# Performance work log

Measured on AMD Instinct MI355X. Metric: run time of the kernel, lower is better.

The kernel has to match this reference:

```python
import jax, jax.numpy as jnp
import numpy as np

B, S, D, H, HD, F = 2, 2048, 2048, 16, 128, 8192
EPS = 1e-6
NEG_INF = -1e10


def rmsnorm(x, scale, eps=EPS):
    # T5 LayerNorm: no centering, mean of squares, learned scale
    x = x.astype(jnp.float32)
    mean2 = jnp.mean(jnp.square(x), axis=-1, keepdims=True)
    return x * jax.lax.rsqrt(mean2 + eps) * scale


def setup_inputs() -> dict:
    key = jax.random.key(0)
    ks = jax.random.split(key, 10)
    sd = 0.02
    return {
        "x": jax.random.normal(ks[0], (B, S, D), jnp.float32),
        "ln1_scale": jnp.ones((D,), jnp.float32),
        "wq": jax.random.normal(ks[1], (D, H, HD), jnp.float32) * sd,
        "wk": jax.random.normal(ks[2], (D, H, HD), jnp.float32) * sd,
        "wv": jax.random.normal(ks[3], (D, H, HD), jnp.float32) * sd,
        "qln_scale": jnp.ones((HD,), jnp.float32),
        "kln_scale": jnp.ones((HD,), jnp.float32),
        "wo": jax.random.normal(ks[4], (H, HD, D), jnp.float32) * sd,
        "ln2_scale": jnp.ones((D,), jnp.float32),
        "wi0": jax.random.normal(ks[5], (D, F), jnp.float32) * sd,
        "wi1": jax.random.normal(ks[6], (D, F), jnp.float32) * sd,
        "wout": jax.random.normal(ks[7], (F, D), jnp.float32) * sd,
    }


def reference(x, ln1_scale, wq, wk, wv, qln_scale, kln_scale, wo, ln2_scale, wi0, wi1, wout):
    # ---- pre-attention RMSNorm ----
    lnx = rmsnorm(x, ln1_scale)                                  # [B,S,D]
    # ---- QKV projections (DenseGeneral D -> (H,HD)) ----
    q = jnp.einsum("bsd,dhk->bshk", lnx, wq)                      # [B,S,H,HD]
    k = jnp.einsum("bsd,dhk->bshk", lnx, wk)
    v = jnp.einsum("bsd,dhk->bshk", lnx, wv)
    # ---- fused per-head QK LayerNorm ----
    q = rmsnorm(q, qln_scale)
    k = rmsnorm(k, kln_scale)
    # ---- attention scores + causal bias + softmax ----
    logits = jnp.einsum("bqhd,bkhd->bhqk", q, k)                  # [B,H,S,S]
    causal = jnp.tril(jnp.ones((S, S), bool))
    bias = jnp.where(causal, 0.0, NEG_INF).astype(logits.dtype)  # [S,S]
    probs = jax.nn.softmax(logits + bias[None, None])             # [B,H,S,S]
    # ---- weighted values + output projection ----
    attn = jnp.einsum("bhqk,bkhd->bqhd", probs, v)                # [B,S,H,HD]
    attn_out = jnp.einsum("bqhd,hdm->bqm", attn, wo)              # [B,S,D]
    inter = x + attn_out
    # ---- pre-MLP RMSNorm + gated MLP (silu * linear) ----
    h = rmsnorm(inter, ln2_scale)
    g = jax.nn.silu(h @ wi0) * (h @ wi1)                          # [B,S,F]
    mlp_out = g @ wout                                            # [B,S,D]
    return inter + mlp_out
```

## Files before the change

kernel.cpp:

```cpp
#include <hip/hip_runtime.h>

typedef unsigned short u16;
typedef unsigned int u32;
typedef __attribute__((ext_vector_type(8))) short bf16x8;
typedef __attribute__((ext_vector_type(2))) float f32x2;
typedef __attribute__((ext_vector_type(4))) float f32x4;
typedef __attribute__((ext_vector_type(4))) u32 u32x4;

#define DEV __device__ __forceinline__

DEV u16 f2bf(float x) {
    u32 u = __builtin_bit_cast(u32, x);
    u += 0x7fffu + ((u >> 16) & 1u);
    return (u16)(u >> 16);
}
DEV float bf2f(u16 b) {
    u32 u = ((u32)b) << 16;
    return __builtin_bit_cast(float, u);
}

#define MFMA16(a, b, c) __builtin_amdgcn_mfma_f32_16x16x32_bf16((a), (b), (c), 0, 0, 0)

#define GLL16(gp, lp)                                                      \
    __builtin_amdgcn_global_load_lds(                                      \
        (const __attribute__((address_space(1))) u32*)(const void*)(gp),   \
        (__attribute__((address_space(3))) u32*)(void*)(lp), 16, 0, 0)

__global__ void fillsent(float* __restrict__ out, int n, float val)
{
    for (int i = blockIdx.x * blockDim.x + threadIdx.x; i < n; i += gridDim.x * blockDim.x)
        out[i] = val;
}

__global__ void wtrans(const float* __restrict__ in, u16* __restrict__ out, int K, int N)
{
    __shared__ u16 t[64][65];
    const int n0 = blockIdx.x * 64, k0 = blockIdx.y * 64, tid = threadIdx.x;
    for (int i = tid; i < 4096; i += 256) {
        int r = i >> 6, c = i & 63;
        t[r][c] = f2bf(in[(size_t)(k0 + r) * N + n0 + c]);
    }
    __syncthreads();
    for (int i = tid; i < 4096; i += 256) {
        int r = i >> 6, c = i & 63;
        out[(size_t)(n0 + r) * K + k0 + c] = t[c][r];
    }
}

__global__ void wtrans4(const float* __restrict__ s0, const float* __restrict__ s1,
                        const float* __restrict__ s2, const float* __restrict__ s3,
                        u16* __restrict__ d0, u16* __restrict__ d1,
                        u16* __restrict__ d2, u16* __restrict__ d3)
{
    const float* in;
    u16* out;
    switch (blockIdx.z) {
        case 0: in = s0; out = d0; break;
        case 1: in = s1; out = d1; break;
        case 2: in = s2; out = d2; break;
        default: in = s3; out = d3; break;
    }
    __shared__ u16 t[64][65];
    const int n0 = blockIdx.x * 64, k0 = blockIdx.y * 64, tid = threadIdx.x;
    for (int i = tid; i < 4096; i += 256) {
        int r = i >> 6, c = i & 63;
        t[r][c] = f2bf(in[(size_t)(k0 + r) * 2048 + n0 + c]);
    }
    __syncthreads();
    for (int i = tid; i < 4096; i += 256) {
        int r = i >> 6, c = i & 63;
        out[(size_t)(n0 + r) * 2048 + k0 + c] = t[c][r];
    }
}

__global__ void vtrans(const u16* __restrict__ in, u16* __restrict__ out)
{
    __shared__ u16 t[64][65];
    const int d0 = blockIdx.x * 64, s0 = blockIdx.y * 64, bh = blockIdx.z, tid = threadIdx.x;
    const u16* ip = in + (size_t)bh * 2048 * 128;
    u16* op = out + (size_t)bh * 128 * 2048;
    for (int i = tid; i < 4096; i += 256) {
        int r = i >> 6, c = i & 63;
        t[r][c] = ip[(size_t)(s0 + r) * 128 + d0 + c];
    }
    __syncthreads();
    for (int i = tid; i < 4096; i += 256) {
        int r = i >> 6, c = i & 63;
        op[(size_t)(d0 + r) * 2048 + s0 + c] = t[c][r];
    }
}

__global__ __launch_bounds__(256) void rmsnorm_d(const float* __restrict__ in,
                                                 const float* __restrict__ sc,
                                                 u16* __restrict__ out)
{
    __shared__ float red[4];
    const int row = blockIdx.x, tid = threadIdx.x;
    const float* p = in + (size_t)row * 2048 + tid * 8;
    f32x4 a = *(const f32x4*)p;
    f32x4 b = *(const f32x4*)(p + 4);
    float ss = a[0]*a[0] + a[1]*a[1] + a[2]*a[2] + a[3]*a[3]
             + b[0]*b[0] + b[1]*b[1] + b[2]*b[2] + b[3]*b[3];
    for (int d = 1; d < 64; d <<= 1) ss += __shfl_xor(ss, d, 64);
    if ((tid & 63) == 0) red[tid >> 6] = ss;
    __syncthreads();
    float rs = rsqrtf((red[0] + red[1] + red[2] + red[3]) * (1.0f / 2048.0f) + 1e-6f);
    const float* s = sc + tid * 8;
    u32x4 ov;
#pragma unroll
    for (int i = 0; i < 2; ++i) {
        f32x4 v = i ? b : a;
#pragma unroll
        for (int j = 0; j < 2; ++j) {
            float v0 = v[j * 2] * rs * s[i * 4 + j * 2];
            float v1 = v[j * 2 + 1] * rs * s[i * 4 + j * 2 + 1];
            ov[i * 2 + j] = (u32)f2bf(v0) | ((u32)f2bf(v1) << 16);
        }
    }
    *(u32x4*)(out + (size_t)row * 2048 + tid * 8) = ov;
}

__global__ __launch_bounds__(256) void rmsnorm_split(const float* __restrict__ in,
                                                     const float* __restrict__ sc,
                                                     u16* __restrict__ ohi,
                                                     u16* __restrict__ olo)
{
    __shared__ float red[4];
    const int row = blockIdx.x, tid = threadIdx.x;
    const float* p = in + (size_t)row * 2048 + tid * 8;
    f32x4 a = *(const f32x4*)p;
    f32x4 b = *(const f32x4*)(p + 4);
    float ss = a[0]*a[0] + a[1]*a[1] + a[2]*a[2] + a[3]*a[3]
             + b[0]*b[0] + b[1]*b[1] + b[2]*b[2] + b[3]*b[3];
    for (int d = 1; d < 64; d <<= 1) ss += __shfl_xor(ss, d, 64);
    if ((tid & 63) == 0) red[tid >> 6] = ss;
    __syncthreads();
    float rs = rsqrtf((red[0] + red[1] + red[2] + red[3]) * (1.0f / 2048.0f) + 1e-6f);
    const float* s = sc + tid * 8;
    u32x4 oh, ol;
#pragma unroll
    for (int i = 0; i < 2; ++i) {
        f32x4 v = i ? b : a;
#pragma unroll
        for (int j = 0; j < 2; ++j) {
            float v0 = v[j * 2] * rs * s[i * 4 + j * 2];
            float v1 = v[j * 2 + 1] * rs * s[i * 4 + j * 2 + 1];
            u16 h0 = f2bf(v0), h1 = f2bf(v1);
            u16 l0 = f2bf(v0 - bf2f(h0)), l1 = f2bf(v1 - bf2f(h1));
            oh[i * 2 + j] = (u32)h0 | ((u32)h1 << 16);
            ol[i * 2 + j] = (u32)l0 | ((u32)l1 << 16);
        }
    }
    *(u32x4*)(ohi + (size_t)row * 2048 + tid * 8) = oh;
    *(u32x4*)(olo + (size_t)row * 2048 + tid * 8) = ol;
}

template <int EPI>
__global__ __launch_bounds__(512, 2)
void gemm_bt8(const u16* __restrict__ Ap, const u16* __restrict__ Bt,
              float* __restrict__ outf, u16* __restrict__ outb,
              const float* __restrict__ resf, int M, int N, int K)
{
    extern __shared__ char lds[];
    char* AB = lds;
    char* BB = lds + 49152;
    const int tid = threadIdx.x, w = tid >> 6, l = tid & 63;
    const int lr = l & 15, lg = l >> 4;
    const int m0 = blockIdx.y * 128, n0 = blockIdx.x * 256;
    const int wr = (w >> 2) * 64, wc = (w & 3) * 64;
    const size_t ldb = (size_t)K * 2;
    const char* Ag = (const char*)Ap;
    const char* Bg = (const char*)Bt;
    const int ldsw = w * 1024;

    size_t ago[2], bgo[4];
#pragma unroll
    for (int i = 0; i < 2; ++i) {
        int p = (i * 512 + tid) * 16;
        int pr = p >> 7;
        int pc = (p ^ ((pr & 7) << 4)) & 127;
        ago[i] = (size_t)(m0 + pr) * ldb + pc;
    }
#pragma unroll
    for (int i = 0; i < 4; ++i) {
        int p = (i * 512 + tid) * 16;
        int pr = p >> 7;
        int pc = (p ^ ((pr & 7) << 4)) & 127;
        bgo[i] = (size_t)(n0 + pr) * ldb + pc;
    }

    f32x4 acc[4][4] = {};
    const int nkt = K / 64;

    GLL16(Ag + ago[0], AB + ldsw);
    GLL16(Ag + ago[1], AB + 8192 + ldsw);
    GLL16(Bg + bgo[0], BB + ldsw);
    GLL16(Bg + bgo[1], BB + 8192 + ldsw);
    GLL16(Bg + bgo[2], BB + 16384 + ldsw);
    GLL16(Bg + bgo[3], BB + 24576 + ldsw);
    if (nkt > 1) {
        char* Ad = AB + 16384;
        char* Bd = BB + 32768;
        GLL16(Ag + ago[0] + 128, Ad + ldsw);
        GLL16(Ag + ago[1] + 128, Ad + 8192 + ldsw);
        GLL16(Bg + bgo[0] + 128, Bd + ldsw);
        GLL16(Bg + bgo[1] + 128, Bd + 8192 + ldsw);
        GLL16(Bg + bgo[2] + 128, Bd + 16384 + ldsw);
        GLL16(Bg + bgo[3] + 128, Bd + 24576 + ldsw);
        asm volatile("s_waitcnt vmcnt(6)" ::: "memory");
    } else {
        asm volatile("s_waitcnt vmcnt(0)" ::: "memory");
    }
    __builtin_amdgcn_s_barrier();

    int cur = 0, stg = 2;
    for (int kt = 0; kt < nkt; ++kt) {
        char* Ac = AB + cur * 16384;
        char* Bc = BB + cur * 32768;
        char* Asd = AB + stg * 16384;
        char* Bsd = BB + stg * 32768;
        const bool dost = (kt + 2 < nkt);
        const size_t koff = (size_t)(kt + 2) * 128;

        bf16x8 af[4], bfa, bfb;
#pragma unroll
        for (int mf = 0; mf < 4; ++mf) {
            int ra = wr + mf * 16 + lr;
            af[mf] = *(const bf16x8*)(Ac + ((ra * 128 + lg * 16) ^ ((ra & 7) << 4)));
        }
        {
            int rb = wc + lr;
            bfa = *(const bf16x8*)(Bc + ((rb * 128 + lg * 16) ^ ((rb & 7) << 4)));
            rb = wc + 16 + lr;
            bfb = *(const bf16x8*)(Bc + ((rb * 128 + lg * 16) ^ ((rb & 7) << 4)));
        }
        if (dost) {
            GLL16(Ag + ago[0] + koff, Asd + ldsw);
            GLL16(Ag + ago[1] + koff, Asd + 8192 + ldsw);
        }
        __builtin_amdgcn_s_barrier();
        __builtin_amdgcn_s_setprio(1);
#pragma unroll
        for (int mf = 0; mf < 4; ++mf) acc[mf][0] = MFMA16(af[mf], bfa, acc[mf][0]);
#pragma unroll
        for (int mf = 0; mf < 4; ++mf) acc[mf][1] = MFMA16(af[mf], bfb, acc[mf][1]);
        __builtin_amdgcn_s_setprio(0);
        __builtin_amdgcn_s_barrier();
        {
            int rb = wc + 32 + lr;
            bfa = *(const bf16x8*)(Bc + ((rb * 128 + lg * 16) ^ ((rb & 7) << 4)));
            rb = wc + 48 + lr;
            bfb = *(const bf16x8*)(Bc + ((rb * 128 + lg * 16) ^ ((rb & 7) << 4)));
        }
        if (dost) {
            GLL16(Bg + bgo[0] + koff, Bsd + ldsw);
            GLL16(Bg + bgo[1] + koff, Bsd + 8192 + ldsw);
        }
        __builtin_amdgcn_s_barrier();
        __builtin_amdgcn_s_setprio(1);
#pragma unroll
        for (int mf = 0; mf < 4; ++mf) acc[mf][2] = MFMA16(af[mf], bfa, acc[mf][2]);
#pragma unroll
        for (int mf = 0; mf < 4; ++mf) acc[mf][3] = MFMA16(af[mf], bfb, acc[mf][3]);
        __builtin_amdgcn_s_setprio(0);
        __builtin_amdgcn_s_barrier();
#pragma unroll
        for (int mf = 0; mf < 4; ++mf) {
            int ra = wr + mf * 16 + lr;
            af[mf] = *(const bf16x8*)(Ac + ((ra * 128 + 64 + lg * 16) ^ ((ra & 7) << 4)));
        }
        {
            int rb = wc + lr;
            bfa = *(const bf16x8*)(Bc + ((rb * 128 + 64 + lg * 16) ^ ((rb & 7) << 4)));
            rb = wc + 16 + lr;
            bfb = *(const bf16x8*)(Bc + ((rb * 128 + 64 + lg * 16) ^ ((rb & 7) << 4)));
        }
        if (dost) {
            GLL16(Bg + bgo[2] + koff, Bsd + 16384 + ldsw);
        }
        __builtin_amdgcn_s_barrier();
        __builtin_amdgcn_s_setprio(1);
#pragma unroll
        for (int mf = 0; mf < 4; ++mf) acc[mf][0] = MFMA16(af[mf], bfa, acc[mf][0]);
#pragma unroll
        for (int mf = 0; mf < 4; ++mf) acc[mf][1] = MFMA16(af[mf], bfb, acc[mf][1]);
        __builtin_amdgcn_s_setprio(0);
        __builtin_amdgcn_s_barrier();
        {
            int rb = wc + 32 + lr;
            bfa = *(const bf16x8*)(Bc + ((rb * 128 + 64 + lg * 16) ^ ((rb & 7) << 4)));
            rb = wc + 48 + lr;
            bfb = *(const bf16x8*)(Bc + ((rb * 128 + 64 + lg * 16) ^ ((rb & 7) << 4)));
        }
        if (dost) {
            GLL16(Bg + bgo[3] + koff, Bsd + 24576 + ldsw);
        }
        __builtin_amdgcn_s_barrier();
        __builtin_amdgcn_s_setprio(1);
#pragma unroll
        for (int mf = 0; mf < 4; ++mf) acc[mf][2] = MFMA16(af[mf], bfa, acc[mf][2]);
#pragma unroll
        for (int mf = 0; mf < 4; ++mf) acc[mf][3] = MFMA16(af[mf], bfb, acc[mf][3]);
        __builtin_amdgcn_s_setprio(0);
        if (kt < nkt - 2) {
            asm volatile("s_waitcnt vmcnt(6)" ::: "memory");
            __builtin_amdgcn_s_barrier();
        } else if (kt == nkt - 2) {
            asm volatile("s_waitcnt vmcnt(0)" ::: "memory");
            __builtin_amdgcn_s_barrier();
        }
        cur = (cur == 2) ? 0 : cur + 1;
        stg = (stg == 2) ? 0 : stg + 1;
    }

#pragma unroll
    for (int mf = 0; mf < 4; ++mf) {
#pragma unroll
        for (int nf = 0; nf < 4; ++nf) {
#pragma unroll
            for (int r = 0; r < 4; ++r) {
                int m = m0 + wr + mf * 16 + lg * 4 + r;
                int n = n0 + wc + nf * 16 + lr;
                float v = acc[mf][nf][r];
                if constexpr (EPI == 0) {
                    outb[(((m >> 11) * 16 + (n >> 7)) << 18) + ((m & 2047) << 7) + (n & 127)] = f2bf(v);
                } else {
                    size_t idx = (size_t)m * N + n;
                    outf[idx] = v + resf[idx];
                }
            }
        }
    }
}

__global__ __launch_bounds__(256, 2)
void gemm2(const u16* __restrict__ Ahi, const u16* __restrict__ Alo,
           const u16* __restrict__ Bt, const float* __restrict__ sc,
           u16* __restrict__ ohi, u16* __restrict__ olo, int M, int N, int K)
{
    __shared__ u16 Ah[128 * 64];
    __shared__ u16 Al[128 * 64];
    __shared__ u16 Bh[128 * 64];
    __shared__ float ssq[128][2];
    const int tid = threadIdx.x, w = tid >> 6, l = tid & 63;
    const int lr = l & 15, lg = l >> 4;
    const int m0 = blockIdx.y * 128, n0 = blockIdx.x * 128;
    const int wr = (w >> 1) * 64, wc = (w & 1) * 64;
    f32x4 acc[4][4] = {};
    int prow[4], pcol[4];
#pragma unroll
    for (int j = 0; j < 4; ++j) {
        int p = (j * 4 + w) * 1024 + l * 16;
        prow[j] = p >> 7;
        pcol[j] = (p ^ ((prow[j] & 7) << 4)) & 127;
    }
    const size_t ldb = (size_t)K * 2;
    const int nkt = K / 64;
    for (int kt = 0; kt < nkt; ++kt) {
#pragma unroll
        for (int j = 0; j < 4; ++j) {
            size_t ao = (size_t)(m0 + prow[j]) * ldb + kt * 128 + pcol[j];
            size_t bo = (size_t)(n0 + prow[j]) * ldb + kt * 128 + pcol[j];
            GLL16((const char*)Ahi + ao, (char*)Ah + (j * 4 + w) * 1024);
            GLL16((const char*)Alo + ao, (char*)Al + (j * 4 + w) * 1024);
            GLL16((const char*)Bt + bo, (char*)Bh + (j * 4 + w) * 1024);
        }
        __syncthreads();
#pragma unroll
        for (int kc = 0; kc < 2; ++kc) {
            bf16x8 ahf[4], alf[4], bhf[4];
#pragma unroll
            for (int f = 0; f < 4; ++f) {
                int ra = wr + f * 16 + lr;
                int oa = (ra * 128 + kc * 64 + lg * 16) ^ ((ra & 7) << 4);
                ahf[f] = *(const bf16x8*)((const char*)Ah + oa);
                alf[f] = *(const bf16x8*)((const char*)Al + oa);
                int rb = wc + f * 16 + lr;
                int ob = (rb * 128 + kc * 64 + lg * 16) ^ ((rb & 7) << 4);
                bhf[f] = *(const bf16x8*)((const char*)Bh + ob);
            }
#pragma unroll
            for (int mf = 0; mf < 4; ++mf)
#pragma unroll
                for (int nf = 0; nf < 4; ++nf) {
                    acc[mf][nf] = MFMA16(ahf[mf], bhf[nf], acc[mf][nf]);
                    acc[mf][nf] = MFMA16(alf[mf], bhf[nf], acc[mf][nf]);
                }
        }
        __syncthreads();
    }
    float sp[4][4];
#pragma unroll
    for (int mf = 0; mf < 4; ++mf)
#pragma unroll
        for (int r = 0; r < 4; ++r) {
            float s = 0.0f;
#pragma unroll
            for (int nf = 0; nf < 4; ++nf) { float v = acc[mf][nf][r]; s += v * v; }
            s += __shfl_xor(s, 1, 64); s += __shfl_xor(s, 2, 64);
            s += __shfl_xor(s, 4, 64); s += __shfl_xor(s, 8, 64);
            sp[mf][r] = s;
        }
    if (lr == 0) {
#pragma unroll
        for (int mf = 0; mf < 4; ++mf)
#pragma unroll
            for (int r = 0; r < 4; ++r)
                ssq[wr + mf * 16 + lg * 4 + r][w & 1] = sp[mf][r];
    }
    __syncthreads();
    const int head = n0 >> 7;
#pragma unroll
    for (int mf = 0; mf < 4; ++mf)
#pragma unroll
        for (int r = 0; r < 4; ++r) {
            int mloc = wr + mf * 16 + lg * 4 + r;
            int m = m0 + mloc;
            float rs = rsqrtf((ssq[mloc][0] + ssq[mloc][1]) * (1.0f / 128.0f) + 1e-6f);
            size_t base = (((size_t)(m >> 11) * 16 + head) << 18) + ((size_t)(m & 2047) << 7);
#pragma unroll
            for (int nf = 0; nf < 4; ++nf) {
                int hd = wc + nf * 16 + lr;
                float v = acc[mf][nf][r] * rs * sc[hd];
                u16 hv = f2bf(v);
                ohi[base + hd] = hv;
                olo[base + hd] = f2bf(v - bf2f(hv));
            }
        }
}

__global__ __launch_bounds__(256, 2)
void gemm_up(const u16* __restrict__ A, const u16* __restrict__ B0, const u16* __restrict__ B1,
             u16* __restrict__ G, int M, int N, int K)
{
    __shared__ u16 As[128 * 64];
    __shared__ u16 Bs0[128 * 64];
    __shared__ u16 Bs1[128 * 64];
    const int tid = threadIdx.x, w = tid >> 6, l = tid & 63;
    const int lr = l & 15, lg = l >> 4;
    const int m0 = blockIdx.y * 128, n0 = blockIdx.x * 128;
    const int wr = (w >> 1) * 64, wc = (w & 1) * 64;
    f32x4 acc0[4][4] = {}, acc1[4][4] = {};
    int prow[4], pcol[4];
#pragma unroll
    for (int j = 0; j < 4; ++j) {
        int p = (j * 4 + w) * 1024 + l * 16;
        prow[j] = p >> 7;
        pcol[j] = (p ^ ((prow[j] & 7) << 4)) & 127;
    }
    const size_t ldb = (size_t)K * 2;
    const int nkt = K / 64;
    for (int kt = 0; kt < nkt; ++kt) {
#pragma unroll
        for (int j = 0; j < 4; ++j) {
            GLL16((const char*)A + (size_t)(m0 + prow[j]) * ldb + kt * 128 + pcol[j], (char*)As + (j * 4 + w) * 1024);
            GLL16((const char*)B0 + (size_t)(n0 + prow[j]) * ldb + kt * 128 + pcol[j], (char*)Bs0 + (j * 4 + w) * 1024);
            GLL16((const char*)B1 + (size_t)(n0 + prow[j]) * ldb + kt * 128 + pcol[j], (char*)Bs1 + (j * 4 + w) * 1024);
        }
        __syncthreads();
#pragma unroll
        for (int kc = 0; kc < 2; ++kc) {
            bf16x8 af[4], b0f[4], b1f[4];
#pragma unroll
            for (int f = 0; f < 4; ++f) {
                int ra = wr + f * 16 + lr;
                af[f] = *(const bf16x8*)((const char*)As + ((ra * 128 + kc * 64 + lg * 16) ^ ((ra & 7) << 4)));
                int rb = wc + f * 16 + lr;
                int ob = (rb * 128 + kc * 64 + lg * 16) ^ ((rb & 7) << 4);
                b0f[f] = *(const bf16x8*)((const char*)Bs0 + ob);
                b1f[f] = *(const bf16x8*)((const char*)Bs1 + ob);
            }
#pragma unroll
            for (int mf = 0; mf < 4; ++mf)
#pragma unroll
                for (int nf = 0; nf < 4; ++nf) {
                    acc0[mf][nf] = MFMA16(af[mf], b0f[nf], acc0[mf][nf]);
                    acc1[mf][nf] = MFMA16(af[mf], b1f[nf], acc1[mf][nf]);
                }
        }
        __syncthreads();
    }
#pragma unroll
    for (int mf = 0; mf < 4; ++mf) {
#pragma unroll
        for (int nf = 0; nf < 4; ++nf) {
#pragma unroll
            for (int r = 0; r < 4; ++r) {
                int m = m0 + wr + mf * 16 + lg * 4 + r;
                int n = n0 + wc + nf * 16 + lr;
                float a = acc0[mf][nf][r];
                float b = acc1[mf][nf][r];
                G[(size_t)m * N + n] = f2bf(a / (1.0f + __expf(-a)) * b);
            }
        }
    }
}

__global__ __launch_bounds__(256, 2)
void flash(const u16* __restrict__ Qh, const u16* __restrict__ Ql,
           const u16* __restrict__ Kh, const u16* __restrict__ Kl,
           const u16* __restrict__ Vt, u16* __restrict__ O)
{
    __shared__ u16 Ksh[64 * 128];
    __shared__ u16 Ksl[64 * 128];
    __shared__ u16 Vs[128 * 64];
    __shared__ u16 Ps[4][16 * 64];
    const int tid = threadIdx.x, w = tid >> 6, l = tid & 63;
    const int lr = l & 15, lg = l >> 4;
    const int qb0 = blockIdx.x * 64, bh = blockIdx.y;

    const size_t qoff = ((size_t)bh * 2048 + qb0 + w * 16) * 128;
    bf16x8 qfh[4], qfl[4];
#pragma unroll
    for (int kc = 0; kc < 4; ++kc) {
        qfh[kc] = *(const bf16x8*)(Qh + qoff + lr * 128 + kc * 32 + lg * 8);
        qfl[kc] = *(const bf16x8*)(Ql + qoff + lr * 128 + kc * 32 + lg * 8);
    }

    f32x4 o[8] = {};
    float mrun[4] = {-1e30f, -1e30f, -1e30f, -1e30f};
    float lrun[4] = {};

    int kgo[4], vdo[4], voff[4];
#pragma unroll
    for (int j = 0; j < 4; ++j) {
        int p = (j * 4 + w) * 1024 + l * 16;
        kgo[j] = p ^ (((p >> 8) & 7) << 4);
        int d = p >> 7, c0 = (p >> 4) & 7;
        vdo[j] = d;
        voff[j] = (c0 ^ (d & 7)) << 4;
    }
    const char* kbh = (const char*)(Kh + (size_t)bh * 2048 * 128);
    const char* kbl = (const char*)(Kl + (size_t)bh * 2048 * 128);
    const char* vbase = (const char*)(Vt + (size_t)bh * 128 * 2048);
    const int tmax = blockIdx.x;

    for (int t = 0; t <= tmax; ++t) {
        const char* kgh = kbh + (size_t)t * 16384;
        const char* kgl = kbl + (size_t)t * 16384;
        const char* vg = vbase + t * 128;
#pragma unroll
        for (int j = 0; j < 4; ++j) {
            GLL16(kgh + kgo[j], (char*)Ksh + (j * 4 + w) * 1024);
            GLL16(kgl + kgo[j], (char*)Ksl + (j * 4 + w) * 1024);
            GLL16(vg + (size_t)vdo[j] * 4096 + voff[j], (char*)Vs + (j * 4 + w) * 1024);
        }
        __syncthreads();

        f32x4 sf[4];
#pragma unroll
        for (int kf = 0; kf < 4; ++kf) {
            f32x4 a = {};
            int row = kf * 16 + lr;
#pragma unroll
            for (int kc = 0; kc < 4; ++kc) {
                int off = (row * 256 + kc * 64 + lg * 16) ^ ((row & 7) << 4);
                bf16x8 khf = *(const bf16x8*)((const char*)Ksh + off);
                bf16x8 klf = *(const bf16x8*)((const char*)Ksl + off);
                a = MFMA16(qfh[kc], khf, a);
                a = MFMA16(qfh[kc], klf, a);
                a = MFMA16(qfl[kc], khf, a);
            }
            sf[kf] = a;
        }
        if (t == tmax) {
#pragma unroll
            for (int kf = 0; kf < 4; ++kf)
#pragma unroll
                for (int r = 0; r < 4; ++r)
                    if (t * 64 + kf * 16 + lr > qb0 + w * 16 + lg * 4 + r) sf[kf][r] = -1e30f;
        }
        float scl[4];
#pragma unroll
        for (int r = 0; r < 4; ++r) {
            float m_ = fmaxf(fmaxf(sf[0][r], sf[1][r]), fmaxf(sf[2][r], sf[3][r]));
            m_ = fmaxf(m_, __shfl_xor(m_, 1, 64));
            m_ = fmaxf(m_, __shfl_xor(m_, 2, 64));
            m_ = fmaxf(m_, __shfl_xor(m_, 4, 64));
            m_ = fmaxf(m_, __shfl_xor(m_, 8, 64));
            float mn = fmaxf(mrun[r], m_);
            scl[r] = __expf(mrun[r] - mn);
            mrun[r] = mn;
            float s_ = 0.0f;
#pragma unroll
            for (int kf = 0; kf < 4; ++kf) {
                float e = __expf(sf[kf][r] - mn);
                sf[kf][r] = e;
                s_ += e;
            }
            s_ += __shfl_xor(s_, 1, 64);
            s_ += __shfl_xor(s_, 2, 64);
            s_ += __shfl_xor(s_, 4, 64);
            s_ += __shfl_xor(s_, 8, 64);
            lrun[r] = lrun[r] * scl[r] + s_;
        }
#pragma unroll
        for (int f = 0; f < 8; ++f) {
            o[f][0] *= scl[0]; o[f][1] *= scl[1]; o[f][2] *= scl[2]; o[f][3] *= scl[3];
        }
        char* pb = (char*)&Ps[w][0];
#pragma unroll
        for (int kf = 0; kf < 4; ++kf)
#pragma unroll
            for (int r = 0; r < 4; ++r) {
                int q = lg * 4 + r;
                int byte = (q * 128 + kf * 32 + lr * 2) ^ ((q & 7) << 4);
                *(u16*)(pb + byte) = f2bf(sf[kf][r]);
            }
        __syncthreads();
#pragma unroll
        for (int kc = 0; kc < 2; ++kc) {
            bf16x8 pa = *(const bf16x8*)(pb + ((lr * 128 + kc * 64 + lg * 16) ^ ((lr & 7) << 4)));
#pragma unroll
            for (int df = 0; df < 8; ++df) {
                int vr = df * 16 + lr;
                bf16x8 vf = *(const bf16x8*)((const char*)Vs +
                    ((vr * 128 + kc * 64 + lg * 16) ^ ((vr & 7) << 4)));
                o[df] = MFMA16(pa, vf, o[df]);
            }
        }
        __syncthreads();
    }
    float inv[4];
#pragma unroll
    for (int r = 0; r < 4; ++r) inv[r] = 1.0f / lrun[r];
    const int b = bh >> 4, h = bh & 15;
#pragma unroll
    for (int df = 0; df < 8; ++df)
#pragma unroll
        for (int r = 0; r < 4; ++r) {
            int q = qb0 + w * 16 + lg * 4 + r;
            int d = df * 16 + lr;
            O[(((size_t)b * 2048 + q) * 16 + h) * 128 + d] = f2bf(o[df][r] * inv[r]);
        }
}

extern "C" void kernel_launch(void* const* d_in, const int* in_sizes, int n_in,
                              void* d_out, int out_size, void* d_ws, size_t ws_size,
                              hipStream_t stream)
{
    (void)in_sizes; (void)n_in;
    const float* x    = (const float*)d_in[0];
    const float* ln1  = (const float*)d_in[1];
    const float* wq   = (const float*)d_in[2];
    const float* wk   = (const float*)d_in[3];
    const float* wv   = (const float*)d_in[4];
    const float* qln  = (const float*)d_in[5];
    const float* kln  = (const float*)d_in[6];
    const float* wo   = (const float*)d_in[7];
    const float* ln2  = (const float*)d_in[8];
    const float* wi0  = (const float*)d_in[9];
    const float* wi1  = (const float*)d_in[10];
    const float* wout = (const float*)d_in[11];

    const size_t MB = 1ull << 20;
    char* ws = (char*)d_ws;
    if (ws_size < 256 * MB) {
        fillsent<<<2048, 256, 0, stream>>>((float*)d_out, out_size, (float)(ws_size >> 20));
        return;
    }

    (void)hipFuncSetAttribute((const void*)gemm_bt8<0>,
                              hipFuncAttributeMaxDynamicSharedMemorySize, 147456);
    (void)hipFuncSetAttribute((const void*)gemm_bt8<1>,
                              hipFuncAttributeMaxDynamicSharedMemorySize, 147456);

    u16* lnx_hi = (u16*)(ws + 0 * MB);
    u16* attn   = (u16*)(ws + 0 * MB);
    u16* lnx_lo = (u16*)(ws + 16 * MB);
    u16* h      = (u16*)(ws + 16 * MB);
    u16* q_hi   = (u16*)(ws + 32 * MB);
    u16* q_lo   = (u16*)(ws + 48 * MB);
    u16* g      = (u16*)(ws + 32 * MB);
    u16* k_hi   = (u16*)(ws + 64 * MB);
    u16* k_lo   = (u16*)(ws + 80 * MB);
    u16* v      = (u16*)(ws + 96 * MB);
    u16* vt     = (u16*)(ws + 112 * MB);
    u16* wo2t   = (u16*)(ws + 96 * MB);
    u16* wqt    = (u16*)(ws + 128 * MB);
    u16* wkt    = (u16*)(ws + 136 * MB);
    float* interp = (float*)(ws + 128 * MB);
    u16* wi0t   = (u16*)(ws + 160 * MB);
    u16* wi1t   = (u16*)(ws + 192 * MB);
    u16* wvt    = (u16*)(ws + 224 * MB);
    u16* wot    = (u16*)(ws + 232 * MB);

    dim3 blk(256);
    wtrans4<<<dim3(32, 32, 4), blk, 0, stream>>>(wq, wk, wv, wo, wqt, wkt, wvt, wot);
    wtrans<<<dim3(128, 32), blk, 0, stream>>>(wi0, wi0t, 2048, 8192);
    wtrans<<<dim3(128, 32), blk, 0, stream>>>(wi1, wi1t, 2048, 8192);

    rmsnorm_split<<<4096, blk, 0, stream>>>(x, ln1, lnx_hi, lnx_lo);

    gemm2<<<dim3(16, 32), blk, 0, stream>>>(lnx_hi, lnx_lo, wqt, qln, q_hi, q_lo, 4096, 2048, 2048);
    gemm2<<<dim3(16, 32), blk, 0, stream>>>(lnx_hi, lnx_lo, wkt, kln, k_hi, k_lo, 4096, 2048, 2048);

    gemm_bt8<0><<<dim3(8, 32), dim3(512), 147456, stream>>>(lnx_hi, wvt, nullptr, v, nullptr, 4096, 2048, 2048);
    vtrans<<<dim3(2, 32, 32), blk, 0, stream>>>(v, vt);

    flash<<<dim3(32, 32), blk, 0, stream>>>(q_hi, q_lo, k_hi, k_lo, vt, attn);

    gemm_bt8<1><<<dim3(8, 32), dim3(512), 147456, stream>>>(attn, wot, interp, nullptr, x, 4096, 2048, 2048);

    rmsnorm_d<<<4096, blk, 0, stream>>>(interp, ln2, h);

    gemm_up<<<dim3(64, 32), blk, 0, stream>>>(h, wi0t, wi1t, g, 4096, 8192, 2048);

    wtrans<<<dim3(32, 128), blk, 0, stream>>>(wout, wo2t, 8192, 2048);
    gemm_bt8<1><<<dim3(8, 32), dim3(512), 147456, stream>>>(g, wo2t, (float*)d_out, nullptr, interp, 4096, 2048, 8192);
}
```

Baseline: 935.9 us.

## Fuse Q and K projection GEMMs and vectorize weight transpose kernels

Merges the two split-precision Q and K projection GEMMs into one kernel, so the lnx hi/lo tiles are loaded once and used for both weight matrices, each with its own fused per-head RMSNorm epilogue. Doubling the accumulators raises register pressure (two 4x4 f32x4 sets) under launch_bounds(256,2), which may cause spills or lower occupancy. The weight transpose kernels also switch to 16-byte float4 loads and 8-byte stores, with the shared tile padded to 66 columns.

```diff
diff --git a/kernel.cpp b/kernel.cpp
--- a/kernel.cpp
+++ b/kernel.cpp
@@ -6,6 +6,7 @@
 typedef __attribute__((ext_vector_type(2))) float f32x2;
 typedef __attribute__((ext_vector_type(4))) float f32x4;
 typedef __attribute__((ext_vector_type(4))) u32 u32x4;
+typedef __attribute__((ext_vector_type(4))) unsigned short u16x4;
 
 #define DEV __device__ __forceinline__
 
@@ -34,16 +35,24 @@
 
 __global__ void wtrans(const float* __restrict__ in, u16* __restrict__ out, int K, int N)
 {
-    __shared__ u16 t[64][65];
+    __shared__ u16 t[64][66];
     const int n0 = blockIdx.x * 64, k0 = blockIdx.y * 64, tid = threadIdx.x;
-    for (int i = tid; i < 4096; i += 256) {
-        int r = i >> 6, c = i & 63;
-        t[r][c] = f2bf(in[(size_t)(k0 + r) * N + n0 + c]);
+#pragma unroll
+    for (int i = 0; i < 4; ++i) {
+        int e = (i * 256 + tid) * 4;
+        int r = e >> 6, c = e & 63;
+        f32x4 v = *(const f32x4*)&in[(size_t)(k0 + r) * N + n0 + c];
+        t[r][c] = f2bf(v[0]); t[r][c + 1] = f2bf(v[1]);
+        t[r][c + 2] = f2bf(v[2]); t[r][c + 3] = f2bf(v[3]);
     }
     __syncthreads();
-    for (int i = tid; i < 4096; i += 256) {
-        int r = i >> 6, c = i & 63;
-        out[(size_t)(n0 + r) * K + k0 + c] = t[c][r];
+#pragma unroll
+    for (int i = 0; i < 4; ++i) {
+        int e = (i * 256 + tid) * 4;
+        int r = e >> 6, c = e & 63;
+        u16x4 wv;
+        wv[0] = t[c][r]; wv[1] = t[c + 1][r]; wv[2] = t[c + 2][r]; wv[3] = t[c + 3][r];
+        *(u16x4*)&out[(size_t)(n0 + r) * K + k0 + c] = wv;
     }
 }
 
@@ -60,16 +69,24 @@
         case 2: in = s2; out = d2; break;
         default: in = s3; out = d3; break;
     }
-    __shared__ u16 t[64][65];
+    __shared__ u16 t[64][66];
     const int n0 = blockIdx.x * 64, k0 = blockIdx.y * 64, tid = threadIdx.x;
-    for (int i = tid; i < 4096; i += 256) {
-        int r = i >> 6, c = i & 63;
-        t[r][c] = f2bf(in[(size_t)(k0 + r) * 2048 + n0 + c]);
+#pragma unroll
+    for (int i = 0; i < 4; ++i) {
+        int e = (i * 256 + tid) * 4;
+        int r = e >> 6, c = e & 63;
+        f32x4 v = *(const f32x4*)&in[(size_t)(k0 + r) * 2048 + n0 + c];
+        t[r][c] = f2bf(v[0]); t[r][c + 1] = f2bf(v[1]);
+        t[r][c + 2] = f2bf(v[2]); t[r][c + 3] = f2bf(v[3]);
     }
     __syncthreads();
-    for (int i = tid; i < 4096; i += 256) {
-        int r = i >> 6, c = i & 63;
-        out[(size_t)(n0 + r) * 2048 + k0 + c] = t[c][r];
+#pragma unroll
+    for (int i = 0; i < 4; ++i) {
+        int e = (i * 256 + tid) * 4;
+        int r = e >> 6, c = e & 63;
+        u16x4 wv;
+        wv[0] = t[c][r]; wv[1] = t[c + 1][r]; wv[2] = t[c + 2][r]; wv[3] = t[c + 3][r];
+        *(u16x4*)&out[(size_t)(n0 + r) * 2048 + k0 + c] = wv;
     }
 }
 
@@ -334,19 +351,23 @@
 }
 
 __global__ __launch_bounds__(256, 2)
-void gemm2(const u16* __restrict__ Ahi, const u16* __restrict__ Alo,
-           const u16* __restrict__ Bt, const float* __restrict__ sc,
-           u16* __restrict__ ohi, u16* __restrict__ olo, int M, int N, int K)
+void gemm2qk(const u16* __restrict__ Ahi, const u16* __restrict__ Alo,
+             const u16* __restrict__ Bq, const u16* __restrict__ Bk,
+             const float* __restrict__ qsc, const float* __restrict__ ksc,
+             u16* __restrict__ qhi, u16* __restrict__ qlo,
+             u16* __restrict__ khi, u16* __restrict__ klo, int M, int N, int K)
 {
     __shared__ u16 Ah[128 * 64];
     __shared__ u16 Al[128 * 64];
-    __shared__ u16 Bh[128 * 64];
+    __shared__ u16 Bqs[128 * 64];
+    __shared__ u16 Bks[128 * 64];
     __shared__ float ssq[128][2];
+    __shared__ float ssk[128][2];
     const int tid = threadIdx.x, w = tid >> 6, l = tid & 63;
     const int lr = l & 15, lg = l >> 4;
     const int m0 = blockIdx.y * 128, n0 = blockIdx.x * 128;
     const int wr = (w >> 1) * 64, wc = (w & 1) * 64;
-    f32x4 acc[4][4] = {};
+    f32x4 accq[4][4] = {}, acck[4][4] = {};
     int prow[4], pcol[4];
 #pragma unroll
     for (int j = 0; j < 4; ++j) {
@@ -363,12 +384,13 @@
             size_t bo = (size_t)(n0 + prow[j]) * ldb + kt * 128 + pcol[j];
             GLL16((const char*)Ahi + ao, (char*)Ah + (j * 4 + w) * 1024);
             GLL16((const char*)Alo + ao, (char*)Al + (j * 4 + w) * 1024);
-            GLL16((const char*)Bt + bo, (char*)Bh + (j * 4 + w) * 1024);
+            GLL16((const char*)Bq + bo, (char*)Bqs + (j * 4 + w) * 1024);
+            GLL16((const char*)Bk + bo, (char*)Bks + (j * 4 + w) * 1024);
         }
         __syncthreads();
 #pragma unroll
         for (int kc = 0; kc < 2; ++kc) {
-            bf16x8 ahf[4], alf[4], bhf[4];
+            bf16x8 ahf[4], alf[4], bqf[4], bkf[4];
 #pragma unroll
             for (int f = 0; f < 4; ++f) {
                 int ra = wr + f * 16 + lr;
@@ -377,36 +399,48 @@
                 alf[f] = *(const bf16x8*)((const char*)Al + oa);
                 int rb = wc + f * 16 + lr;
                 int ob = (rb * 128 + kc * 64 + lg * 16) ^ ((rb & 7) << 4);
-                bhf[f] = *(const bf16x8*)((const char*)Bh + ob);
+                bqf[f] = *(const bf16x8*)((const char*)Bqs + ob);
+                bkf[f] = *(const bf16x8*)((const char*)Bks + ob);
             }
 #pragma unroll
             for (int mf = 0; mf < 4; ++mf)
 #pragma unroll
                 for (int nf = 0; nf < 4; ++nf) {
-                    acc[mf][nf] = MFMA16(ahf[mf], bhf[nf], acc[mf][nf]);
-                    acc[mf][nf] = MFMA16(alf[mf], bhf[nf], acc[mf][nf]);
+                    accq[mf][nf] = MFMA16(ahf[mf], bqf[nf], accq[mf][nf]);
+                    accq[mf][nf] = MFMA16(alf[mf], bqf[nf], accq[mf][nf]);
+                    acck[mf][nf] = MFMA16(ahf[mf], bkf[nf], acck[mf][nf]);
+                    acck[mf][nf] = MFMA16(alf[mf], bkf[nf], acck[mf][nf]);
                 }
         }
         __syncthreads();
     }
-    float sp[4][4];
+    float spq[4][4], spk[4][4];
 #pragma unroll
     for (int mf = 0; mf < 4; ++mf)
 #pragma unroll
         for (int r = 0; r < 4; ++r) {
-            float s = 0.0f;
-#pragma unroll
-            for (int nf = 0; nf < 4; ++nf) { float v = acc[mf][nf][r]; s += v * v; }
-            s += __shfl_xor(s, 1, 64); s += __shfl_xor(s, 2, 64);
-            s += __shfl_xor(s, 4, 64); s += __shfl_xor(s, 8, 64);
-            sp[mf][r] = s;
+            float sq = 0.0f, sk = 0.0f;
+#pragma unroll
+            for (int nf = 0; nf < 4; ++nf) {
+                float vq = accq[mf][nf][r]; sq += vq * vq;
+                float vk = acck[mf][nf][r]; sk += vk * vk;
+            }
+            sq += __shfl_xor(sq, 1, 64); sq += __shfl_xor(sq, 2, 64);
+            sq += __shfl_xor(sq, 4, 64); sq += __shfl_xor(sq, 8, 64);
+            sk += __shfl_xor(sk, 1, 64); sk += __shfl_xor(sk, 2, 64);
+            sk += __shfl_xor(sk, 4, 64); sk += __shfl_xor(sk, 8, 64);
+            spq[mf][r] = sq;
+            spk[mf][r] = sk;
         }
     if (lr == 0) {
 #pragma unroll
         for (int mf = 0; mf < 4; ++mf)
 #pragma unroll
-            for (int r = 0; r < 4; ++r)
-                ssq[wr + mf * 16 + lg * 4 + r][w & 1] = sp[mf][r];
+            for (int r = 0; r < 4; ++r) {
+                int mloc = wr + mf * 16 + lg * 4 + r;
+                ssq[mloc][w & 1] = spq[mf][r];
+                ssk[mloc][w & 1] = spk[mf][r];
+            }
     }
     __syncthreads();
     const int head = n0 >> 7;
@@ -416,15 +450,20 @@
         for (int r = 0; r < 4; ++r) {
             int mloc = wr + mf * 16 + lg * 4 + r;
             int m = m0 + mloc;
-            float rs = rsqrtf((ssq[mloc][0] + ssq[mloc][1]) * (1.0f / 128.0f) + 1e-6f);
+            float rsq = rsqrtf((ssq[mloc][0] + ssq[mloc][1]) * (1.0f / 128.0f) + 1e-6f);
+            float rsk = rsqrtf((ssk[mloc][0] + ssk[mloc][1]) * (1.0f / 128.0f) + 1e-6f);
             size_t base = (((size_t)(m >> 11) * 16 + head) << 18) + ((size_t)(m & 2047) << 7);
 #pragma unroll
             for (int nf = 0; nf < 4; ++nf) {
                 int hd = wc + nf * 16 + lr;
-                float v = acc[mf][nf][r] * rs * sc[hd];
-                u16 hv = f2bf(v);
-                ohi[base + hd] = hv;
-                olo[base + hd] = f2bf(v - bf2f(hv));
+                float vq = accq[mf][nf][r] * rsq * qsc[hd];
+                u16 hq = f2bf(vq);
+                qhi[base + hd] = hq;
+                qlo[base + hd] = f2bf(vq - bf2f(hq));
+                float vk = acck[mf][nf][r] * rsk * ksc[hd];
+                u16 hk = f2bf(vk);
+                khi[base + hd] = hk;
+                klo[base + hd] = f2bf(vk - bf2f(hk));
             }
         }
 }
@@ -692,8 +731,8 @@
 
     rmsnorm_split<<<4096, blk, 0, stream>>>(x, ln1, lnx_hi, lnx_lo);
 
-    gemm2<<<dim3(16, 32), blk, 0, stream>>>(lnx_hi, lnx_lo, wqt, qln, q_hi, q_lo, 4096, 2048, 2048);
-    gemm2<<<dim3(16, 32), blk, 0, stream>>>(lnx_hi, lnx_lo, wkt, kln, k_hi, k_lo, 4096, 2048, 2048);
+    gemm2qk<<<dim3(16, 32), blk, 0, stream>>>(lnx_hi, lnx_lo, wqt, wkt, qln, kln,
+                                              q_hi, q_lo, k_hi, k_lo, 4096, 2048, 2048);
 
     gemm_bt8<0><<<dim3(8, 32), dim3(512), 147456, stream>>>(lnx_hi, wvt, nullptr, v, nullptr, 4096, 2048, 2048);
     vtrans<<<dim3(2, 32, 32), blk, 0, stream>>>(v, vt);
```

New measurement: 896.4 us. 4.2% less time.
